# Kernel tuning notes

Hardware: AMD Instinct MI355X
Metric: run time of the kernel (lower is better)

## Reference

```python
import jax, jax.numpy as jnp
import numpy as np

B, S, IN_DIM, H, NC = 4, 512, 32, 64, 3

def setup_inputs() -> dict:
    key = jax.random.key(0)
    ks = jax.random.split(key, 20)
    def lin(k, i, o):
        bound = 1.0 / np.sqrt(i)
        kw, kb = jax.random.split(k)
        W = jax.random.uniform(kw, (i, o), jnp.float32, -bound, bound)
        b = jax.random.uniform(kb, (o,), jnp.float32, -bound, bound)
        return W, b
    W1, b1 = lin(ks[0], IN_DIM, H)
    W2, b2 = lin(ks[1], H, H)
    We1, be1 = lin(ks[2], 2 * H, H)
    We2, be2 = lin(ks[3], H, H)
    Wd1, bd1 = lin(ks[4], 2 * H, H // 2)
    Wd2, bd2 = lin(ks[5], H // 2, 1)
    Wc1, bc1 = lin(ks[6], 2 * H, 32)
    Wc2, bc2 = lin(ks[7], 32, NC)
    x = jax.random.normal(ks[8], (B, S, IN_DIM), jnp.float32)
    return {"x": x, "W1": W1, "b1": b1, "W2": W2, "b2": b2,
            "We1": We1, "be1": be1, "We2": We2, "be2": be2,
            "Wd1": Wd1, "bd1": bd1, "Wd2": Wd2, "bd2": bd2,
            "Wc1": Wc1, "bc1": bc1, "Wc2": Wc2, "bc2": bc2}

def reference(x, W1, b1, W2, b2, We1, be1, We2, be2,
              Wd1, bd1, Wd2, bd2, Wc1, bc1, Wc2, bc2):
    b, s, _ = x.shape
    # node encoder: Linear -> ReLU -> Linear
    nodes = jax.nn.relu(x @ W1 + b1) @ W2 + b2          # [b,s,H]
    h = nodes.shape[-1]
    # all-pairs concat: pairs[b,i,j] = [nodes[b,i], nodes[b,j]]
    pi = jnp.broadcast_to(nodes[:, :, None, :], (b, s, s, h))
    pj = jnp.broadcast_to(nodes[:, None, :, :], (b, s, s, h))
    pairs = jnp.concatenate([pi, pj], axis=-1)          # [b,s,s,2H]
    # edge network
    raw_msgs = jax.nn.relu(pairs @ We1 + be1) @ We2 + be2   # [b,s,s,H]
    # demon gate
    keep = jax.nn.sigmoid(jax.nn.relu(pairs @ Wd1 + bd1) @ Wd2 + bd2)  # [b,s,s,1]
    active = (raw_msgs * keep).sum(axis=2)              # [b,s,H]
    trash = (raw_msgs * (1.0 - keep)).sum(axis=2)       # [b,s,H]
    main_emb = (nodes + active).mean(axis=1)            # [b,H]
    trash_emb = trash.mean(axis=1)                      # [b,H]
    feat = jnp.concatenate([main_emb, trash_emb], axis=-1)  # [b,2H]
    return jax.nn.relu(feat @ Wc1 + bc1) @ Wc2 + bc2    # [b,NC]
```

## Files before the change

### kernel.cpp

```cpp
#include <hip/hip_runtime.h>

#define BB 4
#define SS 512
#define IND 32
#define HH 64
#define NCC 3

#define IPB 4
#define NPB (BB * 256)
#define NNB 512

#define OFF_U    0
#define OFF_V    (OFF_U + BB*SS*HH)
#define OFF_P    (OFF_V + BB*SS*HH)
#define OFF_QT   (OFF_P + BB*SS*32)
#define OFF_SN   (OFF_QT + 32*BB*SS)
#define OFF_SA   (OFF_SN + NNB*HH)
#define OFF_SH   (OFF_SA + NPB*HH)
#define OFF_SKP  (OFF_SH + NPB*HH)

__device__ __forceinline__ float rl(float v, int l) {
    return __uint_as_float(__builtin_amdgcn_readlane(__float_as_uint(v), l));
}

__global__ __launch_bounds__(256) void k_nodes(
    const float* __restrict__ x,  const float* __restrict__ W1, const float* __restrict__ b1,
    const float* __restrict__ W2, const float* __restrict__ b2,
    const float* __restrict__ We1,const float* __restrict__ be1,
    const float* __restrict__ Wd1,const float* __restrict__ bd1,
    float* __restrict__ ws)
{
    float* U = ws + OFF_U;  float* V4 = ws + OFF_V;
    float* P = ws + OFF_P;  float* Qt4 = ws + OFF_QT;
    float* SN = ws + OFF_SN;
    __shared__ float sn_lds[4][64];
    const int tid = threadIdx.x, wave = tid >> 6, lane = tid & 63;
    const int L = ((blockIdx.x & 7) << 6) | (blockIdx.x >> 3);
    const int node = L * 4 + wave;

    float xv = (lane < IND) ? x[node * IND + lane] : 0.0f;
    float h1 = b1[lane];
    #pragma unroll
    for (int k = 0; k < IND; k++)
        h1 = fmaf(__shfl(xv, k, 64), W1[k * HH + lane], h1);
    h1 = fmaxf(h1, 0.0f);

    float nd = b2[lane];
    #pragma unroll 16
    for (int k = 0; k < HH; k++)
        nd = fmaf(__shfl(h1, k, 64), W2[k * HH + lane], nd);

    float uv = be1[lane];
    float vv = 0.0f;
    float pq = (lane < 32) ? bd1[lane] : 0.0f;
    const float* WdCol = (lane < 32) ? (Wd1 + lane) : (Wd1 + HH * 32 + (lane - 32));
    #pragma unroll 16
    for (int k = 0; k < HH; k++) {
        float s = __shfl(nd, k, 64);
        uv = fmaf(s, We1[k * HH + lane], uv);
        vv = fmaf(s, We1[(HH + k) * HH + lane], vv);
        pq = fmaf(s, WdCol[k * 32], pq);
    }
    U[node * HH + lane] = uv;
    V4[(L * 64 + lane) * 4 + wave] = vv;
    if (lane < 32) {
        P[node * 32 + lane] = pq;
    } else {
        int k = lane - 32;
        Qt4[((k >> 2) * (BB * SS) + node) * 4 + (k & 3)] = pq;
    }

    sn_lds[wave][lane] = nd;
    __syncthreads();
    if (tid < 64)
        SN[L * 64 + tid] = (sn_lds[0][tid] + sn_lds[1][tid]) + (sn_lds[2][tid] + sn_lds[3][tid]);
}

__global__ __launch_bounds__(256, 4) void k_pairs(
    const float* __restrict__ wd2, const float* __restrict__ bd2,
    float* __restrict__ ws)
{
    const float*  U   = ws + OFF_U;
    const float4* V4  = (const float4*)(ws + OFF_V);
    const float*  P   = ws + OFF_P;
    const float4* Qt4 = (const float4*)(ws + OFF_QT);
    float* SA = ws + OFF_SA;  float* SHo = ws + OFF_SH;  float* SKp = ws + OFF_SKP;

    __shared__ float4 gs[4][64];
    __shared__ float redA[4][64], redH[4][64], redK[4];

    const int tid = threadIdx.x, wave = tid >> 6, lane = tid & 63;
    const int d   = blockIdx.x;
    const int xcd = d & 7;
    const int b   = xcd >> 1;
    const int jc  = xcd & 1;
    const int ic  = d >> 3;
    const int i0  = ic * IPB;
    const int lidx = (b << 8) | (ic << 1) | jc;
    const int jbase = b * SS + jc * 256 + wave * 64;

    const float4* Qp = Qt4 + jbase + lane;
    const float4* Vp = V4 + (jbase >> 2) * 64 + lane;
    float4 q[8], v[16];
    #pragma unroll
    for (int kg = 0; kg < 8; kg++) q[kg] = Qp[kg * (BB * SS)];
    #pragma unroll
    for (int jq = 0; jq < 8; jq++) v[jq] = Vp[jq * 64];

    const float u0 = U[(b * SS + i0 + 0) * HH + lane];
    const float u1 = U[(b * SS + i0 + 1) * HH + lane];
    const float u2 = U[(b * SS + i0 + 2) * HH + lane];
    const float u3 = U[(b * SS + i0 + 3) * HH + lane];
    const float pk0 = P[(b * SS + i0 + 0) * 32 + (lane & 31)];
    const float pk1 = P[(b * SS + i0 + 1) * 32 + (lane & 31)];
    const float pk2 = P[(b * SS + i0 + 2) * 32 + (lane & 31)];
    const float pk3 = P[(b * SS + i0 + 3) * 32 + (lane & 31)];
    const float wv  = wd2[lane & 31];
    const float bd2v = bd2[0];

    float a0 = bd2v, a1 = bd2v, a2 = bd2v, a3 = bd2v;
    #pragma unroll
    for (int kg = 0; kg < 8; kg++) {
        #pragma unroll
        for (int t = 0; t < 4; t++) {
            const int k = kg * 4 + t;
            float qv = (t == 0) ? q[kg].x : (t == 1) ? q[kg].y : (t == 2) ? q[kg].z : q[kg].w;
            float w  = rl(wv, k);
            a0 = fmaf(w, fmaxf(rl(pk0, k) + qv, 0.0f), a0);
            a1 = fmaf(w, fmaxf(rl(pk1, k) + qv, 0.0f), a1);
            a2 = fmaf(w, fmaxf(rl(pk2, k) + qv, 0.0f), a2);
            a3 = fmaf(w, fmaxf(rl(pk3, k) + qv, 0.0f), a3);
        }
    }
    float g0 = 1.0f / (1.0f + __expf(-a0));
    float g1 = 1.0f / (1.0f + __expf(-a1));
    float g2 = 1.0f / (1.0f + __expf(-a2));
    float g3 = 1.0f / (1.0f + __expf(-a3));
    float sk = (g0 + g1) + (g2 + g3);
    gs[wave][lane] = make_float4(g0, g1, g2, g3);

    #pragma unroll
    for (int jq = 8; jq < 16; jq++) v[jq] = Vp[jq * 64];
    __builtin_amdgcn_wave_barrier();

    float sa = 0.0f, sh = 0.0f;
    #pragma unroll
    for (int jq = 0; jq < 16; jq++) {
        #pragma unroll
        for (int t = 0; t < 4; t++) {
            float vv = (t == 0) ? v[jq].x : (t == 1) ? v[jq].y : (t == 2) ? v[jq].z : v[jq].w;
            float4 g4 = gs[wave][jq * 4 + t];
            float h0 = fmaxf(u0 + vv, 0.0f);
            float h1 = fmaxf(u1 + vv, 0.0f);
            float h2 = fmaxf(u2 + vv, 0.0f);
            float h3 = fmaxf(u3 + vv, 0.0f);
            sh += (h0 + h1) + (h2 + h3);
            sa = fmaf(g4.x, h0, sa);
            sa = fmaf(g4.y, h1, sa);
            sa = fmaf(g4.z, h2, sa);
            sa = fmaf(g4.w, h3, sa);
        }
    }

    redA[wave][lane] = sa;
    redH[wave][lane] = sh;
    #pragma unroll
    for (int off = 32; off; off >>= 1) sk += __shfl_xor(sk, off, 64);
    if (lane == 0) redK[wave] = sk;
    __syncthreads();

    if (tid < 64) {
        SA[lidx * 64 + tid]  = (redA[0][tid] + redA[1][tid]) + (redA[2][tid] + redA[3][tid]);
        SHo[lidx * 64 + tid] = (redH[0][tid] + redH[1][tid]) + (redH[2][tid] + redH[3][tid]);
        if (tid == 0)
            SKp[lidx * 16] = (redK[0] + redK[1]) + (redK[2] + redK[3]);
    }
}

__global__ __launch_bounds__(256) void k_final(
    const float* __restrict__ We2, const float* __restrict__ be2,
    const float* __restrict__ Wc1, const float* __restrict__ bc1,
    const float* __restrict__ Wc2, const float* __restrict__ bc2,
    const float* __restrict__ ws, float* __restrict__ out)
{
    const float4* SN4 = (const float4*)(ws + OFF_SN);
    const float4* SA4 = (const float4*)(ws + OFF_SA);
    const float4* SH4 = (const float4*)(ws + OFF_SH);
    const float*  SKp = ws + OFF_SKP;
    __shared__ float4 r4[3][16][16];
    __shared__ float redS[256], saL[64], shL[64];
    __shared__ float featL[128], c1L[32];
    const int tid = threadIdx.x, wave = tid >> 6, lane = tid & 63;
    const int grp = tid >> 4, l16 = tid & 15;
    const int b = blockIdx.x;

    float4 sn4 = make_float4(0.f, 0.f, 0.f, 0.f);
    float4 sa4 = sn4, sh4 = sn4;
    #pragma unroll
    for (int r = 0; r < 8; r++) {
        float4 t = SN4[(b * 128 + r * 16 + grp) * 16 + l16];
        sn4.x += t.x; sn4.y += t.y; sn4.z += t.z; sn4.w += t.w;
    }
    #pragma unroll
    for (int r = 0; r < 16; r++) {
        float4 t = SA4[(b * 256 + r * 16 + grp) * 16 + l16];
        float4 u = SH4[(b * 256 + r * 16 + grp) * 16 + l16];
        sa4.x += t.x; sa4.y += t.y; sa4.z += t.z; sa4.w += t.w;
        sh4.x += u.x; sh4.y += u.y; sh4.z += u.z; sh4.w += u.w;
    }
    r4[0][grp][l16] = sn4;  r4[1][grp][l16] = sa4;  r4[2][grp][l16] = sh4;
    redS[tid] = SKp[(b * 256 + tid) * 16];
    __syncthreads();

    if (wave == 0) {
        const int li = lane >> 2, comp = lane & 3;
        float snT = 0.f, saF = 0.f, shF = 0.f;
        #pragma unroll
        for (int g = 0; g < 16; g++) {
            snT += ((const float*)&r4[0][g][li])[comp];
            saF += ((const float*)&r4[1][g][li])[comp];
            shF += ((const float*)&r4[2][g][li])[comp];
        }
        float skp = (redS[lane] + redS[64 + lane]) + (redS[128 + lane] + redS[192 + lane]);
        #pragma unroll
        for (int off = 32; off; off >>= 1) skp += __shfl_xor(skp, off, 64);
        saL[lane] = saF;  shL[lane] = shF;

        float as = skp * be2[lane];
        float ts = (262144.0f - skp) * be2[lane];
        #pragma unroll 8
        for (int k = 0; k < HH; k++) {
            float w = We2[k * HH + lane];
            float sak = saL[k];
            as = fmaf(sak, w, as);
            ts = fmaf(shL[k] - sak, w, ts);
        }
        featL[lane]      = (snT + as) * (1.0f / 512.0f);
        featL[64 + lane] = ts * (1.0f / 512.0f);
    }
    __syncthreads();

    if (tid < 32) {
        float c1 = bc1[tid];
        #pragma unroll 8
        for (int k = 0; k < 128; k++)
            c1 = fmaf(featL[k], Wc1[k * 32 + tid], c1);
        c1L[tid] = fmaxf(c1, 0.0f);
    }
    __syncthreads();
    if (tid < NCC) {
        float o = bc2[tid];
        #pragma unroll
        for (int k = 0; k < 32; k++)
            o = fmaf(c1L[k], Wc2[k * NCC + tid], o);
        out[b * NCC + tid] = o;
    }
}

extern "C" void kernel_launch(void* const* d_in, const int* in_sizes, int n_in,
                              void* d_out, int out_size, void* d_ws, size_t ws_size,
                              hipStream_t stream) {
    const float* x   = (const float*)d_in[0];
    const float* W1  = (const float*)d_in[1];
    const float* b1  = (const float*)d_in[2];
    const float* W2  = (const float*)d_in[3];
    const float* b2  = (const float*)d_in[4];
    const float* We1 = (const float*)d_in[5];
    const float* be1 = (const float*)d_in[6];
    const float* We2 = (const float*)d_in[7];
    const float* be2 = (const float*)d_in[8];
    const float* Wd1 = (const float*)d_in[9];
    const float* bd1 = (const float*)d_in[10];
    const float* wd2 = (const float*)d_in[11];
    const float* bd2 = (const float*)d_in[12];
    const float* Wc1 = (const float*)d_in[13];
    const float* bc1 = (const float*)d_in[14];
    const float* Wc2 = (const float*)d_in[15];
    const float* bc2 = (const float*)d_in[16];
    float* ws  = (float*)d_ws;
    float* out = (float*)d_out;

    k_nodes<<<dim3(NNB), dim3(256), 0, stream>>>(x, W1, b1, W2, b2, We1, be1, Wd1, bd1, ws);
    k_pairs<<<dim3(NPB), dim3(256), 0, stream>>>(wd2, bd2, ws);
    k_final<<<dim3(BB), dim3(256), 0, stream>>>(We2, be2, Wc1, bc1, Wc2, bc2, ws, out);
}
```

Baseline: 33.50 us.

## Fuse final reduction into pairs kernel via last-block atomic counters

Removes the separate k_final launch. The final per-batch reduction and classifier head now run inside the pairs kernel, in whichever block is last to finish for that batch. Completion is detected with two-level agent-scope atomic ticket counters, and partial sums are written and read through relaxed atomic stores and loads. This saves a launch and its inter-kernel gap. In exchange it adds LDS and atomic traffic to every block, and it relies on the counters (never reset, checked modulo) and on relaxed ordering staying correct across calls.

```diff
diff --git a/kernel.cpp b/kernel.cpp
--- a/kernel.cpp
+++ b/kernel.cpp
@@ -18,9 +18,19 @@
 #define OFF_SA   (OFF_SN + NNB*HH)
 #define OFF_SH   (OFF_SA + NPB*HH)
 #define OFF_SKP  (OFF_SH + NPB*HH)
+#define OFF_T1   (OFF_SKP + NPB*16)
+#define OFF_T2   (OFF_T1 + 128)
+
+#define AGENT __HIP_MEMORY_SCOPE_AGENT
 
 __device__ __forceinline__ float rl(float v, int l) {
     return __uint_as_float(__builtin_amdgcn_readlane(__float_as_uint(v), l));
+}
+__device__ __forceinline__ void ast(float* p, float v) {
+    __hip_atomic_store(p, v, __ATOMIC_RELAXED, AGENT);
+}
+__device__ __forceinline__ float ald(const float* p) {
+    return __hip_atomic_load((float*)p, __ATOMIC_RELAXED, AGENT);
 }
 
 __global__ __launch_bounds__(256) void k_nodes(
@@ -76,18 +86,26 @@
         SN[L * 64 + tid] = (sn_lds[0][tid] + sn_lds[1][tid]) + (sn_lds[2][tid] + sn_lds[3][tid]);
 }
 
-__global__ __launch_bounds__(256, 4) void k_pairs(
+__global__ __launch_bounds__(256, 4) void k_pairs_final(
     const float* __restrict__ wd2, const float* __restrict__ bd2,
-    float* __restrict__ ws)
+    const float* __restrict__ We2, const float* __restrict__ be2,
+    const float* __restrict__ Wc1, const float* __restrict__ bc1,
+    const float* __restrict__ Wc2, const float* __restrict__ bc2,
+    float* __restrict__ ws, float* __restrict__ out)
 {
     const float*  U   = ws + OFF_U;
     const float4* V4  = (const float4*)(ws + OFF_V);
     const float*  P   = ws + OFF_P;
     const float4* Qt4 = (const float4*)(ws + OFF_QT);
     float* SA = ws + OFF_SA;  float* SHo = ws + OFF_SH;  float* SKp = ws + OFF_SKP;
+    unsigned int* tick1 = (unsigned int*)(ws + OFF_T1);
+    unsigned int* tick2 = (unsigned int*)(ws + OFF_T2);
 
     __shared__ float4 gs[4][64];
     __shared__ float redA[4][64], redH[4][64], redK[4];
+    __shared__ int lastFlag;
+    __shared__ float4 r4[3][16][16];
+    __shared__ float redS[256], saL[64], shL[64], featL[128], c1L[32];
 
     const int tid = threadIdx.x, wave = tid >> 6, lane = tid & 63;
     const int d   = blockIdx.x;
@@ -170,90 +188,94 @@
     __syncthreads();
 
     if (tid < 64) {
-        SA[lidx * 64 + tid]  = (redA[0][tid] + redA[1][tid]) + (redA[2][tid] + redA[3][tid]);
-        SHo[lidx * 64 + tid] = (redH[0][tid] + redH[1][tid]) + (redH[2][tid] + redH[3][tid]);
+        float av = (redA[0][tid] + redA[1][tid]) + (redA[2][tid] + redA[3][tid]);
+        float hv = (redH[0][tid] + redH[1][tid]) + (redH[2][tid] + redH[3][tid]);
+        ast(&SA[lidx * 64 + tid], av);
+        ast(&SHo[lidx * 64 + tid], hv);
         if (tid == 0)
-            SKp[lidx * 16] = (redK[0] + redK[1]) + (redK[2] + redK[3]);
-    }
-}
-
-__global__ __launch_bounds__(256) void k_final(
-    const float* __restrict__ We2, const float* __restrict__ be2,
-    const float* __restrict__ Wc1, const float* __restrict__ bc1,
-    const float* __restrict__ Wc2, const float* __restrict__ bc2,
-    const float* __restrict__ ws, float* __restrict__ out)
-{
-    const float4* SN4 = (const float4*)(ws + OFF_SN);
-    const float4* SA4 = (const float4*)(ws + OFF_SA);
-    const float4* SH4 = (const float4*)(ws + OFF_SH);
-    const float*  SKp = ws + OFF_SKP;
-    __shared__ float4 r4[3][16][16];
-    __shared__ float redS[256], saL[64], shL[64];
-    __shared__ float featL[128], c1L[32];
-    const int tid = threadIdx.x, wave = tid >> 6, lane = tid & 63;
-    const int grp = tid >> 4, l16 = tid & 15;
-    const int b = blockIdx.x;
-
-    float4 sn4 = make_float4(0.f, 0.f, 0.f, 0.f);
-    float4 sa4 = sn4, sh4 = sn4;
-    #pragma unroll
-    for (int r = 0; r < 8; r++) {
-        float4 t = SN4[(b * 128 + r * 16 + grp) * 16 + l16];
-        sn4.x += t.x; sn4.y += t.y; sn4.z += t.z; sn4.w += t.w;
-    }
-    #pragma unroll
-    for (int r = 0; r < 16; r++) {
-        float4 t = SA4[(b * 256 + r * 16 + grp) * 16 + l16];
-        float4 u = SH4[(b * 256 + r * 16 + grp) * 16 + l16];
-        sa4.x += t.x; sa4.y += t.y; sa4.z += t.z; sa4.w += t.w;
-        sh4.x += u.x; sh4.y += u.y; sh4.z += u.z; sh4.w += u.w;
-    }
-    r4[0][grp][l16] = sn4;  r4[1][grp][l16] = sa4;  r4[2][grp][l16] = sh4;
-    redS[tid] = SKp[(b * 256 + tid) * 16];
+            ast(&SKp[lidx * 16], (redK[0] + redK[1]) + (redK[2] + redK[3]));
+    }
     __syncthreads();
 
-    if (wave == 0) {
-        const int li = lane >> 2, comp = lane & 3;
-        float snT = 0.f, saF = 0.f, shF = 0.f;
+    if (tid == 0) {
+        int last = 0;
+        unsigned int o1 = __hip_atomic_fetch_add(&tick1[(xcd << 4) | (ic >> 3)], 1u,
+                                                 __ATOMIC_RELAXED, AGENT);
+        if ((o1 & 7u) == 7u) {
+            unsigned int o2 = __hip_atomic_fetch_add(&tick2[b], 1u,
+                                                     __ATOMIC_RELAXED, AGENT);
+            last = ((o2 & 31u) == 31u);
+        }
+        lastFlag = last;
+    }
+    __syncthreads();
+
+    if (lastFlag) {
+        const float4* SN4 = (const float4*)(ws + OFF_SN);
+        const int grp = tid >> 4, l16 = tid & 15;
+
+        float4 sn4 = make_float4(0.f, 0.f, 0.f, 0.f);
+        float4 sa4 = sn4, sh4 = sn4;
         #pragma unroll
-        for (int g = 0; g < 16; g++) {
-            snT += ((const float*)&r4[0][g][li])[comp];
-            saF += ((const float*)&r4[1][g][li])[comp];
-            shF += ((const float*)&r4[2][g][li])[comp];
-        }
-        float skp = (redS[lane] + redS[64 + lane]) + (redS[128 + lane] + redS[192 + lane]);
+        for (int r = 0; r < 8; r++) {
+            float4 t = SN4[(b * 128 + r * 16 + grp) * 16 + l16];
+            sn4.x += t.x; sn4.y += t.y; sn4.z += t.z; sn4.w += t.w;
+        }
         #pragma unroll
-        for (int off = 32; off; off >>= 1) skp += __shfl_xor(skp, off, 64);
-        saL[lane] = saF;  shL[lane] = shF;
-
-        float as = skp * be2[lane];
-        float ts = (262144.0f - skp) * be2[lane];
-        #pragma unroll 8
-        for (int k = 0; k < HH; k++) {
-            float w = We2[k * HH + lane];
-            float sak = saL[k];
-            as = fmaf(sak, w, as);
-            ts = fmaf(shL[k] - sak, w, ts);
-        }
-        featL[lane]      = (snT + as) * (1.0f / 512.0f);
-        featL[64 + lane] = ts * (1.0f / 512.0f);
-    }
-    __syncthreads();
-
-    if (tid < 32) {
-        float c1 = bc1[tid];
-        #pragma unroll 8
-        for (int k = 0; k < 128; k++)
-            c1 = fmaf(featL[k], Wc1[k * 32 + tid], c1);
-        c1L[tid] = fmaxf(c1, 0.0f);
-    }
-    __syncthreads();
-    if (tid < NCC) {
-        float o = bc2[tid];
-        #pragma unroll
-        for (int k = 0; k < 32; k++)
-            o = fmaf(c1L[k], Wc2[k * NCC + tid], o);
-        out[b * NCC + tid] = o;
+        for (int r = 0; r < 16; r++) {
+            const int rb = (b * 256 + r * 16 + grp) * 64 + l16 * 4;
+            sa4.x += ald(&SA[rb + 0]); sa4.y += ald(&SA[rb + 1]);
+            sa4.z += ald(&SA[rb + 2]); sa4.w += ald(&SA[rb + 3]);
+            sh4.x += ald(&SHo[rb + 0]); sh4.y += ald(&SHo[rb + 1]);
+            sh4.z += ald(&SHo[rb + 2]); sh4.w += ald(&SHo[rb + 3]);
+        }
+        r4[0][grp][l16] = sn4;  r4[1][grp][l16] = sa4;  r4[2][grp][l16] = sh4;
+        redS[tid] = ald(&SKp[(b * 256 + tid) * 16]);
+        __syncthreads();
+
+        if (wave == 0) {
+            const int li = lane >> 2, comp = lane & 3;
+            float snT = 0.f, saF = 0.f, shF = 0.f;
+            #pragma unroll
+            for (int g = 0; g < 16; g++) {
+                snT += ((const float*)&r4[0][g][li])[comp];
+                saF += ((const float*)&r4[1][g][li])[comp];
+                shF += ((const float*)&r4[2][g][li])[comp];
+            }
+            float skp = (redS[lane] + redS[64 + lane]) + (redS[128 + lane] + redS[192 + lane]);
+            #pragma unroll
+            for (int off = 32; off; off >>= 1) skp += __shfl_xor(skp, off, 64);
+            saL[lane] = saF;  shL[lane] = shF;
+
+            float as = skp * be2[lane];
+            float ts = (262144.0f - skp) * be2[lane];
+            #pragma unroll 8
+            for (int k = 0; k < HH; k++) {
+                float w = We2[k * HH + lane];
+                float sak = saL[k];
+                as = fmaf(sak, w, as);
+                ts = fmaf(shL[k] - sak, w, ts);
+            }
+            featL[lane]      = (snT + as) * (1.0f / 512.0f);
+            featL[64 + lane] = ts * (1.0f / 512.0f);
+        }
+        __syncthreads();
+
+        if (tid < 32) {
+            float c1 = bc1[tid];
+            #pragma unroll 8
+            for (int k = 0; k < 128; k++)
+                c1 = fmaf(featL[k], Wc1[k * 32 + tid], c1);
+            c1L[tid] = fmaxf(c1, 0.0f);
+        }
+        __syncthreads();
+        if (tid < NCC) {
+            float o = bc2[tid];
+            #pragma unroll
+            for (int k = 0; k < 32; k++)
+                o = fmaf(c1L[k], Wc2[k * NCC + tid], o);
+            out[b * NCC + tid] = o;
+        }
     }
 }
 
@@ -281,6 +303,6 @@
     float* out = (float*)d_out;
 
     k_nodes<<<dim3(NNB), dim3(256), 0, stream>>>(x, W1, b1, W2, b2, We1, be1, Wd1, bd1, ws);
-    k_pairs<<<dim3(NPB), dim3(256), 0, stream>>>(wd2, bd2, ws);
-    k_final<<<dim3(BB), dim3(256), 0, stream>>>(We2, be2, Wc1, bc1, Wc2, bc2, ws, out);
-}
+    k_pairs_final<<<dim3(NPB), dim3(256), 0, stream>>>(wd2, bd2, We2, be2,
+                                                       Wc1, bc1, Wc2, bc2, ws, out);
+}
```

Result: slower. 36.14 us (+7.9%).
